# Kernel optimization log

Measured on AMD Instinct MI355X. Metric: run time of the kernel, lower is better.

The kernel has to match this reference:

```python
import jax, jax.numpy as jnp
import numpy as np
from jax import lax

B, H, W = 8, 500, 500
M = 2048          # per-image cap on active bottleneck voxels (ragged -> fixed)
GRID = 125        # bottleneck grid size
ENC_RANGE = 125.0
HEADS, ATTN_CH, CH = 4, 128, 64
EPS = 1e-5
NEG = -1e9

def _conv(x, w, b, stride, pad):
    y = lax.conv_general_dilated(x, w, (stride, stride), pad,
                                 dimension_numbers=('NCHW', 'HWIO', 'NCHW'))
    return y + b[None, :, None, None]

def _maxpool2(m):
    return lax.reduce_window(m, -jnp.inf, lax.max, (1, 1, 2, 2), (1, 1, 2, 2), 'VALID')

def setup_inputs():
    key = jax.random.key(0)
    ks = jax.random.split(key, 12)
    occ = (jax.random.uniform(ks[0], (B, 1, H, W)) < 0.005).astype(jnp.float32)
    x = jax.random.normal(ks[1], (B, 1, H, W), dtype=jnp.float32) * occ
    def rn(k, shape, scale):
        return jax.random.normal(k, shape, dtype=jnp.float32) * scale
    return {
        'x': x,
        'w0': rn(ks[2], (3, 3, 1, 32), 0.3), 'b0': jnp.zeros(32, jnp.float32),
        'g0': jnp.ones(32, jnp.float32), 'be0': jnp.zeros(32, jnp.float32),
        'w1': rn(ks[3], (2, 2, 32, 64), 0.1), 'b1': jnp.zeros(64, jnp.float32),
        'g1': jnp.ones(64, jnp.float32), 'be1': jnp.zeros(64, jnp.float32),
        'w2': rn(ks[4], (2, 2, 64, 64), 0.08), 'b2': jnp.zeros(64, jnp.float32),
        'g2': jnp.ones(64, jnp.float32), 'be2': jnp.zeros(64, jnp.float32),
        'wpe': rn(ks[5], (2, 2, CH), 0.5), 'bpe': jnp.zeros((2, CH), jnp.float32),
        'wq': rn(ks[6], (2, CH, ATTN_CH), 0.12), 'bq': jnp.zeros((2, ATTN_CH), jnp.float32),
        'wk': rn(ks[7], (2, CH, ATTN_CH), 0.12), 'bk': jnp.zeros((2, ATTN_CH), jnp.float32),
        'wv': rn(ks[8], (2, CH, ATTN_CH), 0.12), 'bv': jnp.zeros((2, ATTN_CH), jnp.float32),
        'wo': rn(ks[9], (2, ATTN_CH, CH), 0.09), 'bo': jnp.zeros((2, CH), jnp.float32),
        'wh': rn(ks[10], (CH, 4), 0.12), 'bh': jnp.zeros(4, jnp.float32),
    }

def reference(x, w0, b0, g0, be0, w1, b1, g1, be1, w2, b2, g2, be2,
              wpe, bpe, wq, bq, wk, bk, wv, bv, wo, bo, wh, bh):
    # active-site mask (Voxels.from_dense)
    mask0 = (x != 0).any(axis=1, keepdims=True).astype(x.dtype)   # [B,1,500,500]

    def bn_relu(y, g, be):
        # eval-mode BatchNorm1d over active voxel features (running stats 0/1)
        return jax.nn.relu(g[None, :, None, None] * y / jnp.sqrt(1.0 + EPS)
                           + be[None, :, None, None])

    # enc0: submanifold 3x3/s1 -> active set unchanged; inactive inputs are zero
    y = bn_relu(_conv(x, w0, b0, 1, 'SAME'), g0, be0) * mask0
    # enc1/enc2: strided 2x2/s2 -> output active iff any input in window active
    mask1 = _maxpool2(mask0)
    y = bn_relu(_conv(y, w1, b1, 2, 'VALID'), g1, be1) * mask1
    mask2 = _maxpool2(mask1)
    y = bn_relu(_conv(y, w2, b2, 2, 'VALID'), g2, be2) * mask2    # [B,64,125,125]

    # gather active bottleneck voxels per image (ragged -> fixed M + validity mask)
    mflat = mask2.reshape(B, GRID * GRID)
    vals, idx = lax.top_k(mflat, M)     # active-first; stable tie-break (lowest idx)
    valid = vals                        # [B,M] in {0,1}
    feats = jnp.take_along_axis(
        y.reshape(B, CH, GRID * GRID).transpose(0, 2, 1),
        idx[:, :, None], axis=1)        # [B,M,64]
    pos = jnp.stack([idx // GRID, idx % GRID], axis=-1).astype(x.dtype) / ENC_RANGE

    dh = ATTN_CH // HEADS
    kmask = (1.0 - valid)[:, None, None, :] * NEG
    for i in range(2):  # N_ATTN structurally distinct layers
        pe = pos @ wpe[i] + bpe[i]
        h = feats + pe
        q = (h @ wq[i] + bq[i]).reshape(B, M, HEADS, dh)
        k = (h @ wk[i] + bk[i]).reshape(B, M, HEADS, dh)
        v = (h @ wv[i] + bv[i]).reshape(B, M, HEADS, dh)
        s = jnp.einsum('bqhd,bkhd->bhqk', q, k) / jnp.sqrt(jnp.asarray(dh, x.dtype))
        a = jax.nn.softmax(s + kmask, axis=-1)
        o = jnp.einsum('bhqk,bkhd->bqhd', a, v).reshape(B, M, ATTN_CH)
        feats = (feats + o @ wo[i] + bo[i]) * valid[..., None]

    # sparse_global_avg_pool: mean over active voxels per image
    counts = jnp.clip(valid.sum(axis=1, keepdims=True), 1.0, None)
    pooled = feats.sum(axis=1) / counts                            # [B,64]
    return pooled @ wh + bh                                        # [B,4]
```

## Files before the change

kernel.cpp:

```cpp
#include <hip/hip_runtime.h>

#define BDIM   8
#define NPIX   250000
#define G1N    62500
#define G2N    15625
#define NB0    977
#define NB1    245
#define NB2    62
#define CAP0   4096
#define CAP1   4096
#define CAPM   2048
#define CH     64
#define ACH    128
#define NHEADS 4
#define DH     32
#define KSPLIT 4

static constexpr float BN_INV    = 0.99999500003749969f;
static constexpr float ATT_SCALE = 0.17677669529663687f;

typedef _Float16 f16x8 __attribute__((ext_vector_type(8)));
typedef float f32x4 __attribute__((ext_vector_type(4)));

static constexpr size_t E_MAP0  = 0;
static constexpr size_t E_MAP1  = E_MAP0 + (size_t)BDIM*NPIX;
static constexpr size_t E_CNT   = E_MAP1 + (size_t)BDIM*G1N;
static constexpr size_t E_ZEND  = E_CNT + 32;
static constexpr size_t E_BC    = E_ZEND;
static constexpr size_t E_BO    = E_BC + (size_t)3*BDIM*1024;
static constexpr size_t E_BM    = E_BO + (size_t)3*BDIM*1024;
static constexpr size_t E_LIST0 = E_BM + (size_t)3*BDIM*1024*8;
static constexpr size_t E_LIST1 = E_LIST0 + (size_t)BDIM*CAP0;
static constexpr size_t E_LIST2 = E_LIST1 + (size_t)BDIM*CAP1;
static constexpr size_t E_Y0    = E_LIST2 + (size_t)BDIM*CAPM;
static constexpr size_t E_Y1    = E_Y0 + (size_t)BDIM*CAP0*32;
static constexpr size_t E_FE    = E_Y1 + (size_t)BDIM*CAP1*64;
static constexpr size_t E_QF    = E_FE + (size_t)BDIM*CAPM*64;
static constexpr size_t E_KF    = E_QF + (size_t)32*CAPM*32/2;
static constexpr size_t E_VT    = E_KF + (size_t)32*CAPM*32/2;
static constexpr size_t E_PACC  = E_VT + (size_t)32*CAPM*32/2;
static constexpr size_t E_PML   = E_PACC + (size_t)32*CAPM*KSPLIT*32;
static constexpr size_t E_PART  = E_PML + (size_t)32*CAPM*KSPLIT*2;


__device__ __forceinline__ bool act0(const float* x, int pix, int b) {
  return (pix < NPIX) && (x[(size_t)b * NPIX + pix] != 0.f);
}
__device__ __forceinline__ bool act1(const int* map0, int p, int b) {
  if (p >= G1N) return false;
  int i = p / 250, j = p - i * 250;
  const int* m = map0 + (size_t)b * NPIX + (2 * i) * 500 + 2 * j;
  return (m[0] | m[1] | m[500] | m[501]) != 0;
}
__device__ __forceinline__ bool act2(const int* map1, int p, int b) {
  if (p >= G2N) return false;
  int i = p / 125, j = p - i * 125;
  const int* m = map1 + (size_t)b * G1N + (2 * i) * 250 + 2 * j;
  return (m[0] | m[1] | m[250] | m[251]) != 0;
}

#define COUNT_BODY(ACT_EXPR)                                            \
  int idx = blockIdx.x * 256 + threadIdx.x;                             \
  int b = blockIdx.y;                                                   \
  bool act = (ACT_EXPR);                                                \
  unsigned long long mask = __ballot(act);                              \
  __shared__ int wc[4];                                                 \
  if ((threadIdx.x & 63) == 0) {                                        \
    wc[threadIdx.x >> 6] = __popcll(mask);                              \
    bm[((size_t)b * 1024 + blockIdx.x) * 4 + (threadIdx.x >> 6)] = mask;\
  }                                                                     \
  __syncthreads();                                                      \
  if (threadIdx.x == 0)                                                 \
    bcnt[b * 1024 + blockIdx.x] = wc[0] + wc[1] + wc[2] + wc[3];

__global__ void k_cnt0(const float* __restrict__ x, int* __restrict__ bcnt,
                       unsigned long long* __restrict__ bm) {
  COUNT_BODY(act0(x, idx, b))
}
__global__ void k_cnt1(const int* __restrict__ map0, int* __restrict__ bcnt,
                       unsigned long long* __restrict__ bm) {
  COUNT_BODY(act1(map0, idx, b))
}
__global__ void k_cnt2(const int* __restrict__ map1, int* __restrict__ bcnt,
                       unsigned long long* __restrict__ bm) {
  COUNT_BODY(act2(map1, idx, b))
}

__global__ __launch_bounds__(256) void k_scan(const int* __restrict__ bcnt,
                                              int* __restrict__ boff,
                                              int* __restrict__ cnt,
                                              int nblk, int cbase) {
  int b = blockIdx.x;
  int t = threadIdx.x;
  int base = t * 4;
  int v[4];
  int ts = 0;
#pragma unroll
  for (int u = 0; u < 4; ++u) {
    v[u] = (base + u < nblk) ? bcnt[b * 1024 + base + u] : 0;
    ts += v[u];
  }
  int lane = t & 63, w = t >> 6;
  int incl = ts;
#pragma unroll
  for (int off = 1; off < 64; off <<= 1) {
    int o = __shfl_up(incl, off, 64);
    if (lane >= off) incl += o;
  }
  __shared__ int wsum[4];
  if (lane == 63) wsum[w] = incl;
  __syncthreads();
  int woff = 0;
#pragma unroll
  for (int k = 0; k < 3; ++k) if (k < w) woff += wsum[k];
  int run = woff + incl - ts;
#pragma unroll
  for (int u = 0; u < 4; ++u) {
    if (base + u < nblk) boff[b * 1024 + base + u] = run;
    run += v[u];
  }
  if (t == 255) cnt[cbase + b] = run;
}

#define EMIT_PROLOG                                                     \
  int idx = blockIdx.x * 256 + threadIdx.x;                             \
  int b = blockIdx.y;                                                   \
  int lane = threadIdx.x & 63;                                          \
  unsigned long long mask =                                             \
      bm[((size_t)b * 1024 + blockIdx.x) * 4 + (threadIdx.x >> 6)];     \
  bool act = (mask >> lane) & 1;                                        \
  __shared__ int wbase[4];                                              \
  if (lane == 0) wbase[threadIdx.x >> 6] = __popcll(mask);              \
  __syncthreads();                                                      \
  if (threadIdx.x == 0) {                                               \
    int s = boff[b * 1024 + blockIdx.x];                                \
    for (int w = 0; w < 4; ++w) { int c = wbase[w]; wbase[w] = s; s += c; } \
  }                                                                     \
  __syncthreads();                                                      \
  int slot = wbase[threadIdx.x >> 6] + __popcll(mask & ((1ull << lane) - 1ull));

__global__ void k_emit0(const unsigned long long* __restrict__ bm,
                        const int* __restrict__ boff,
                        int* __restrict__ map0, int* __restrict__ list0) {
  EMIT_PROLOG
  if (act && slot < CAP0) {
    list0[b * CAP0 + slot] = idx;
    map0[(size_t)b * NPIX + idx] = slot + 1;
  }
}
__global__ void k_emit1(const unsigned long long* __restrict__ bm,
                        const int* __restrict__ boff,
                        int* __restrict__ map1, int* __restrict__ list1) {
  EMIT_PROLOG
  if (act && slot < CAP1) {
    list1[b * CAP1 + slot] = idx;
    map1[(size_t)b * G1N + idx] = slot + 1;
  }
}
__global__ void k_emit2(const unsigned long long* __restrict__ bm,
                        const int* __restrict__ boff,
                        int* __restrict__ list2) {
  EMIT_PROLOG
  if (act && slot < CAPM) list2[b * CAPM + slot] = idx;
}


__global__ void k_y0(const float* __restrict__ x, const float* __restrict__ w0,
                     const float* __restrict__ b0, const float* __restrict__ g0,
                     const float* __restrict__ be0,
                     const int* __restrict__ list0, const int* __restrict__ cnt,
                     float* __restrict__ y0) {
  int t = blockIdx.x * 256 + threadIdx.x;
  int b = t >> 17;
  int r = t & 131071;
  int slot = r >> 5, c = r & 31;
  int n = min(cnt[b], CAP0);
  if (slot >= n) return;
  int pix = list0[b * CAP0 + slot];
  int i = pix / 500, j = pix - i * 500;
  float acc = b0[c];
#pragma unroll
  for (int di = 0; di < 3; ++di) {
    int ii = i + di - 1;
    if ((unsigned)ii >= 500u) continue;
#pragma unroll
    for (int dj = 0; dj < 3; ++dj) {
      int jj = j + dj - 1;
      if ((unsigned)jj >= 500u) continue;
      acc += x[(size_t)b * NPIX + ii * 500 + jj] * w0[(di * 3 + dj) * 32 + c];
    }
  }
  float o = g0[c] * acc * BN_INV + be0[c];
  y0[((size_t)(b * CAP0) + slot) * 32 + c] = fmaxf(o, 0.f);
}

__global__ void k_y1(const float* __restrict__ y0, const float* __restrict__ w1,
                     const float* __restrict__ b1, const float* __restrict__ g1,
                     const float* __restrict__ be1,
                     const int* __restrict__ map0, const int* __restrict__ list1,
                     const int* __restrict__ cnt, float* __restrict__ y1) {
  int b = blockIdx.x >> 9;
  int sblk = blockIdx.x & 511;
  int s0 = sblk * 8;
  int n = min(cnt[BDIM + b], CAP1);
  if (s0 >= n) return;
  __shared__ float inT[4][32][8];
  for (int idx = threadIdx.x; idx < 1024; idx += 64) {
    int s = idx & 7;
    int r = idx >> 3;
    int ci = r & 31, pp = r >> 5;
    float v = 0.f;
    int sg = s0 + s;
    if (sg < n) {
      int p = list1[b * CAP1 + sg];
      int i = p / 250, j = p - i * 250;
      int sm = map0[(size_t)b * NPIX + (2 * i + (pp >> 1)) * 500 + (2 * j + (pp & 1))];
      if (sm) v = y0[((size_t)(b * CAP0) + (sm - 1)) * 32 + ci];
    }
    inT[pp][ci][s] = v;
  }
  __syncthreads();
  int co = threadIdx.x;
  float acc[8];
#pragma unroll
  for (int s = 0; s < 8; ++s) acc[s] = b1[co];
#pragma unroll 2
  for (int pp = 0; pp < 4; ++pp)
    for (int ci = 0; ci < 32; ++ci) {
      float wv = w1[((pp << 5) + ci) * 64 + co];
      float4 i0 = *(const float4*)&inT[pp][ci][0];
      float4 i1 = *(const float4*)&inT[pp][ci][4];
      acc[0] += i0.x * wv; acc[1] += i0.y * wv; acc[2] += i0.z * wv; acc[3] += i0.w * wv;
      acc[4] += i1.x * wv; acc[5] += i1.y * wv; acc[6] += i1.z * wv; acc[7] += i1.w * wv;
    }
  int smax = min(8, n - s0);
  for (int s = 0; s < smax; ++s) {
    float o = g1[co] * acc[s] * BN_INV + be1[co];
    y1[((size_t)(b * CAP1) + s0 + s) * 64 + co] = fmaxf(o, 0.f);
  }
}

__global__ void k_y2(const float* __restrict__ y1, const float* __restrict__ w2,
                     const float* __restrict__ b2, const float* __restrict__ g2,
                     const float* __restrict__ be2,
                     const int* __restrict__ map1, const int* __restrict__ list2,
                     const int* __restrict__ cnt, float* __restrict__ feats) {
  int b = blockIdx.x >> 8;
  int sblk = blockIdx.x & 255;
  int s0 = sblk * 8;
  int n = min(cnt[2 * BDIM + b], CAPM);
  if (s0 >= n) return;
  __shared__ float inT[4][64][8];
  for (int idx = threadIdx.x; idx < 2048; idx += 64) {
    int s = idx & 7;
    int r = idx >> 3;
    int ci = r & 63, pp = r >> 6;
    float v = 0.f;
    int sg = s0 + s;
    if (sg < n) {
      int p = list2[b * CAPM + sg];
      int i = p / 125, j = p - i * 125;
      int sm = map1[(size_t)b * G1N + (2 * i + (pp >> 1)) * 250 + (2 * j + (pp & 1))];
      if (sm) v = y1[((size_t)(b * CAP1) + (sm - 1)) * 64 + ci];
    }
    inT[pp][ci][s] = v;
  }
  __syncthreads();
  int co = threadIdx.x;
  float acc[8];
#pragma unroll
  for (int s = 0; s < 8; ++s) acc[s] = b2[co];
#pragma unroll 2
  for (int pp = 0; pp < 4; ++pp)
    for (int ci = 0; ci < 64; ++ci) {
      float wv = w2[((pp << 6) + ci) * 64 + co];
      float4 i0 = *(const float4*)&inT[pp][ci][0];
      float4 i1 = *(const float4*)&inT[pp][ci][4];
      acc[0] += i0.x * wv; acc[1] += i0.y * wv; acc[2] += i0.z * wv; acc[3] += i0.w * wv;
      acc[4] += i1.x * wv; acc[5] += i1.y * wv; acc[6] += i1.z * wv; acc[7] += i1.w * wv;
    }
  int smax = min(8, n - s0);
  for (int s = 0; s < smax; ++s) {
    float o = g2[co] * acc[s] * BN_INV + be2[co];
    feats[((size_t)(b * CAPM) + s0 + s) * 64 + co] = fmaxf(o, 0.f);
  }
}


__global__ void k_qkv(const float* __restrict__ feats, const int* __restrict__ list2,
                      const int* __restrict__ cnt,
                      const float* __restrict__ wpe, const float* __restrict__ bpe,
                      const float* __restrict__ wq, const float* __restrict__ bq,
                      const float* __restrict__ wk, const float* __restrict__ bk,
                      const float* __restrict__ wv, const float* __restrict__ bv,
                      int layer, _Float16* __restrict__ qf, _Float16* __restrict__ kf,
                      _Float16* __restrict__ vt) {
  int b = blockIdx.x & 7;
  int sblk = blockIdx.x >> 3;
  int s0 = sblk * 8;
  int n = min(cnt[2 * BDIM + b], CAPM);
  if (s0 >= n) return;
  __shared__ float hT[64][8];
  for (int idx = threadIdx.x; idx < 512; idx += 128) {
    int s = idx & 7, c = idx >> 3;
    float hv = 0.f;
    int sg = s0 + s;
    if (sg < n) {
      int p = list2[b * CAPM + sg];
      int i = p / 125, j = p - i * 125;
      hv = feats[((size_t)(b * CAPM) + sg) * 64 + c]
         + (float)i * (1.f / 125.f) * wpe[(layer * 2 + 0) * 64 + c]
         + (float)j * (1.f / 125.f) * wpe[(layer * 2 + 1) * 64 + c]
         + bpe[layer * 64 + c];
    }
    hT[c][s] = hv;
  }
  __syncthreads();
  int o = threadIdx.x;
  float accq[8], acck[8], accv[8];
  float bqv = bq[layer * 128 + o], bkv = bk[layer * 128 + o], bvv = bv[layer * 128 + o];
#pragma unroll
  for (int s = 0; s < 8; ++s) { accq[s] = bqv; acck[s] = bkv; accv[s] = bvv; }
  const float* wq_ = wq + (size_t)layer * 64 * 128 + o;
  const float* wk_ = wk + (size_t)layer * 64 * 128 + o;
  const float* wv_ = wv + (size_t)layer * 64 * 128 + o;
  for (int c = 0; c < 64; ++c) {
    float wqv = wq_[c * 128], wkv = wk_[c * 128], wvv = wv_[c * 128];
    float4 h0 = *(const float4*)&hT[c][0];
    float4 h1 = *(const float4*)&hT[c][4];
    float hh[8] = {h0.x, h0.y, h0.z, h0.w, h1.x, h1.y, h1.z, h1.w};
#pragma unroll
    for (int s = 0; s < 8; ++s) {
      accq[s] += hh[s] * wqv; acck[s] += hh[s] * wkv; accv[s] += hh[s] * wvv;
    }
  }
  int hd = o >> 5, d = o & 31;
  size_t bh = (size_t)(b * NHEADS + hd);
  int smax = min(8, n - s0);
  for (int s = 0; s < smax; ++s) {
    size_t rb = (bh * CAPM + s0 + s) * 32 + d;
    qf[rb] = (_Float16)accq[s];
    kf[rb] = (_Float16)acck[s];
    vt[(bh * 32 + d) * CAPM + s0 + s] = (_Float16)accv[s];
  }
}


union U4H8 { uint4 u; f16x8 h; };
union PKU  { _Float16 h[2]; unsigned int u; };

#define LOADK(K0, K1, K2, K3, T0)                                          \
  K0 = *(const f16x8*)(kf + (bh + (T0) + qr) * 32 + g8);                   \
  K1 = *(const f16x8*)(kf + (bh + (T0) + 16 + qr) * 32 + g8);              \
  K2 = *(const f16x8*)(kf + (bh + (T0) + 32 + qr) * 32 + g8);              \
  K3 = *(const f16x8*)(kf + (bh + (T0) + 48 + qr) * 32 + g8);

#define LOADV(V0, V1, V2, V3, T0)                                          \
  V0 = *(const f16x8*)(vbase + (size_t)qr * CAPM + (T0) + g8);             \
  V1 = *(const f16x8*)(vbase + (size_t)(16 + qr) * CAPM + (T0) + g8);      \
  V2 = *(const f16x8*)(vbase + (size_t)qr * CAPM + (T0) + 32 + g8);        \
  V3 = *(const f16x8*)(vbase + (size_t)(16 + qr) * CAPM + (T0) + 32 + g8);

#define PROCESS(K0, K1, K2, K3, V0, V1, V2, V3, T0)                        \
  {                                                                        \
    f32x4 z = {0.f, 0.f, 0.f, 0.f};                                        \
    f32x4 st0 = __builtin_amdgcn_mfma_f32_16x16x32_f16(K0, fq, z, 0, 0, 0);\
    f32x4 st1 = __builtin_amdgcn_mfma_f32_16x16x32_f16(K1, fq, z, 0, 0, 0);\
    f32x4 st2 = __builtin_amdgcn_mfma_f32_16x16x32_f16(K2, fq, z, 0, 0, 0);\
    f32x4 st3 = __builtin_amdgcn_mfma_f32_16x16x32_f16(K3, fq, z, 0, 0, 0);\
    if ((T0) + 64 > n) {                                                   \
      _Pragma("unroll") for (int r = 0; r < 4; ++r) {                      \
        if ((T0) + 4 * g + r >= n)      st0[r] = -1e30f;                   \
        if ((T0) + 16 + 4 * g + r >= n) st1[r] = -1e30f;                   \
        if ((T0) + 32 + 4 * g + r >= n) st2[r] = -1e30f;                   \
        if ((T0) + 48 + 4 * g + r >= n) st3[r] = -1e30f;                   \
      }                                                                    \
    }                                                                      \
    float tm = st0[0];                                                     \
    _Pragma("unroll") for (int r = 1; r < 4; ++r) tm = fmaxf(tm, st0[r]);  \
    _Pragma("unroll") for (int r = 0; r < 4; ++r) tm = fmaxf(tm, st1[r]);  \
    _Pragma("unroll") for (int r = 0; r < 4; ++r) tm = fmaxf(tm, st2[r]);  \
    _Pragma("unroll") for (int r = 0; r < 4; ++r) tm = fmaxf(tm, st3[r]);  \
    tm = fmaxf(tm, __shfl_xor(tm, 16));                                    \
    tm = fmaxf(tm, __shfl_xor(tm, 32));                                    \
    float mn = fmaxf(m, tm * ATT_SCALE);                                   \
    float f_ = __expf(m - mn);                                             \
    m = mn;                                                                \
    float ls = 0.f;                                                        \
    {                                                                      \
      PKU a, c;                                                            \
      a.h[0] = (_Float16)__expf(st0[0] * ATT_SCALE - mn);                  \
      a.h[1] = (_Float16)__expf(st0[1] * ATT_SCALE - mn);                  \
      c.h[0] = (_Float16)__expf(st0[2] * ATT_SCALE - mn);                  \
      c.h[1] = (_Float16)__expf(st0[3] * ATT_SCALE - mn);                  \
      ls += (float)a.h[0] + (float)a.h[1] + (float)c.h[0] + (float)c.h[1]; \
      P[(qr * 32 + 0 + 2 * g) ^ swz] = a.u;                                \
      P[(qr * 32 + 1 + 2 * g) ^ swz] = c.u;                                \
      a.h[0] = (_Float16)__expf(st1[0] * ATT_SCALE - mn);                  \
      a.h[1] = (_Float16)__expf(st1[1] * ATT_SCALE - mn);                  \
      c.h[0] = (_Float16)__expf(st1[2] * ATT_SCALE - mn);                  \
      c.h[1] = (_Float16)__expf(st1[3] * ATT_SCALE - mn);                  \
      ls += (float)a.h[0] + (float)a.h[1] + (float)c.h[0] + (float)c.h[1]; \
      P[(qr * 32 + 8 + 2 * g) ^ swz] = a.u;                                \
      P[(qr * 32 + 9 + 2 * g) ^ swz] = c.u;                                \
      a.h[0] = (_Float16)__expf(st2[0] * ATT_SCALE - mn);                  \
      a.h[1] = (_Float16)__expf(st2[1] * ATT_SCALE - mn);                  \
      c.h[0] = (_Float16)__expf(st2[2] * ATT_SCALE - mn);                  \
      c.h[1] = (_Float16)__expf(st2[3] * ATT_SCALE - mn);                  \
      ls += (float)a.h[0] + (float)a.h[1] + (float)c.h[0] + (float)c.h[1]; \
      P[(qr * 32 + 16 + 2 * g) ^ swz] = a.u;                               \
      P[(qr * 32 + 17 + 2 * g) ^ swz] = c.u;                               \
      a.h[0] = (_Float16)__expf(st3[0] * ATT_SCALE - mn);                  \
      a.h[1] = (_Float16)__expf(st3[1] * ATT_SCALE - mn);                  \
      c.h[0] = (_Float16)__expf(st3[2] * ATT_SCALE - mn);                  \
      c.h[1] = (_Float16)__expf(st3[3] * ATT_SCALE - mn);                  \
      ls += (float)a.h[0] + (float)a.h[1] + (float)c.h[0] + (float)c.h[1]; \
      P[(qr * 32 + 24 + 2 * g) ^ swz] = a.u;                               \
      P[(qr * 32 + 25 + 2 * g) ^ swz] = c.u;                               \
    }                                                                      \
    ls += __shfl_xor(ls, 16);                                              \
    ls += __shfl_xor(ls, 32);                                              \
    l = l * f_ + ls;                                                       \
    __builtin_amdgcn_sched_barrier(0);                                     \
    U4H8 pa0, pa1;                                                         \
    pa0.u = *(const uint4*)&P[(qr * 32 + 4 * g) ^ swz];                    \
    pa1.u = *(const uint4*)&P[(qr * 32 + 16 + 4 * g) ^ swz];               \
    float fr0 = __shfl(f_, 4 * g + 0, 16);                                 \
    float fr1 = __shfl(f_, 4 * g + 1, 16);                                 \
    float fr2 = __shfl(f_, 4 * g + 2, 16);                                 \
    float fr3 = __shfl(f_, 4 * g + 3, 16);                                 \
    acc0[0] *= fr0; acc0[1] *= fr1; acc0[2] *= fr2; acc0[3] *= fr3;        \
    acc1[0] *= fr0; acc1[1] *= fr1; acc1[2] *= fr2; acc1[3] *= fr3;        \
    acc0 = __builtin_amdgcn_mfma_f32_16x16x32_f16(pa0.h, V0, acc0, 0, 0, 0);\
    acc1 = __builtin_amdgcn_mfma_f32_16x16x32_f16(pa0.h, V1, acc1, 0, 0, 0);\
    acc0 = __builtin_amdgcn_mfma_f32_16x16x32_f16(pa1.h, V2, acc0, 0, 0, 0);\
    acc1 = __builtin_amdgcn_mfma_f32_16x16x32_f16(pa1.h, V3, acc1, 0, 0, 0);\
  }

__global__ __launch_bounds__(64, 4) void k_attn(
    const _Float16* __restrict__ qf, const _Float16* __restrict__ kf,
    const _Float16* __restrict__ vt, const int* __restrict__ cnt,
    float* __restrict__ pacc, float* __restrict__ pml) {
  int b  = blockIdx.x & 7;
  int rr = blockIdx.x >> 3;
  int qt = rr & 127;
  rr >>= 7;
  int h  = rr & 3;
  int ks = rr >> 2;
  int n = min(cnt[2 * BDIM + b], CAPM);
  int q0 = qt * 16;
  if (q0 >= n) return;
  int lane = threadIdx.x;
  int g = lane >> 4, qr = lane & 15;
  int g8 = g * 8;
  size_t bh = (size_t)(b * NHEADS + h) * CAPM;
  const _Float16* vbase = vt + (size_t)(b * NHEADS + h) * 32 * CAPM;
  f16x8 fq = *(const f16x8*)(qf + (bh + q0 + qr) * 32 + g8);
  f32x4 acc0 = {0.f, 0.f, 0.f, 0.f}, acc1 = {0.f, 0.f, 0.f, 0.f};
  float m = -1e30f, l = 0.f;
  __shared__ unsigned int P[512];
  int swz = (qr & 7) << 2;

  int nt = (n + 63) >> 6;
  int tpc = (nt + KSPLIT - 1) / KSPLIT;
  int tb = ks * tpc, te = min(nt, tb + tpc);
  if (tb < te) {
    f16x8 ka0, ka1, ka2, ka3, va0, va1, va2, va3;
    f16x8 kb0, kb1, kb2, kb3, vb0, vb1, vb2, vb3;
    LOADK(ka0, ka1, ka2, ka3, tb * 64)
    LOADV(va0, va1, va2, va3, tb * 64)
    for (int t = tb; t < te; t += 2) {
      if (t + 1 < te) {
        LOADK(kb0, kb1, kb2, kb3, (t + 1) * 64)
        LOADV(vb0, vb1, vb2, vb3, (t + 1) * 64)
      }
      PROCESS(ka0, ka1, ka2, ka3, va0, va1, va2, va3, t * 64)
      if (t + 1 < te) {
        if (t + 2 < te) {
          LOADK(ka0, ka1, ka2, ka3, (t + 2) * 64)
          LOADV(va0, va1, va2, va3, (t + 2) * 64)
        }
        PROCESS(kb0, kb1, kb2, kb3, vb0, vb1, vb2, vb3, (t + 1) * 64)
      }
    }
  }
#pragma unroll
  for (int r = 0; r < 4; ++r) {
    int tok = q0 + 4 * g + r;
    if (tok < n) {
      float* pp = pacc + ((bh + tok) * KSPLIT + ks) * 32;
      pp[qr] = acc0[r];
      pp[16 + qr] = acc1[r];
    }
  }
  if (g == 0) {
    int tok = q0 + qr;
    if (tok < n) {
      float* pm = pml + ((bh + tok) * KSPLIT + ks) * 2;
      pm[0] = m; pm[1] = l;
    }
  }
}


__global__ __launch_bounds__(256) void k_cproj(
    const float* __restrict__ pacc, const float* __restrict__ pml,
    const float* __restrict__ wo, const float* __restrict__ bo,
    const int* __restrict__ cnt, int layer, float* __restrict__ feats) {
  int b = blockIdx.x & 7;
  int sblk = blockIdx.x >> 3;
  int s0 = sblk * 4;
  int n = min(cnt[2 * BDIM + b], CAPM);
  if (s0 >= n) return;
  __shared__ float oT[128][4];
  __shared__ float wgt[4][4][4];
  __shared__ float invL[4][4];
  int t = threadIdx.x;
  if (t < 16) {
    int s = t >> 2, h = t & 3;
    const float* pm = pml + (((size_t)(b * NHEADS + h) * CAPM + s0 + s) * KSPLIT) * 2;
    float m0 = pm[0], l0 = pm[1];
    float m1 = pm[2], l1 = pm[3];
    float m2 = pm[4], l2 = pm[5];
    float m3 = pm[6], l3 = pm[7];
    float M = fmaxf(fmaxf(m0, m1), fmaxf(m2, m3));
    float w0_ = __expf(m0 - M), w1_ = __expf(m1 - M);
    float w2_ = __expf(m2 - M), w3_ = __expf(m3 - M);
    float L = w0_ * l0 + w1_ * l1 + w2_ * l2 + w3_ * l3;
    wgt[s][h][0] = w0_; wgt[s][h][1] = w1_;
    wgt[s][h][2] = w2_; wgt[s][h][3] = w3_;
    invL[s][h] = 1.f / L;
  }
  __syncthreads();
#pragma unroll
  for (int k = 0; k < 2; ++k) {
    int id = t + k * 256;
    int c = id >> 2, s = id & 3;
    int h = c >> 5, d = c & 31;
    const float* pp = pacc + (((size_t)(b * NHEADS + h) * CAPM + s0 + s) * KSPLIT) * 32 + d;
    float v = pp[0]  * wgt[s][h][0] + pp[32] * wgt[s][h][1]
            + pp[64] * wgt[s][h][2] + pp[96] * wgt[s][h][3];
    oT[c][s] = v * invL[s][h];
  }
  __syncthreads();
  int s = t >> 6, co = t & 63;
  float acc = bo[layer * 64 + co];
  const float* w = wo + (size_t)layer * 128 * 64 + co;
#pragma unroll 8
  for (int c = 0; c < 128; ++c) acc += oT[c][s] * w[c * 64];
  int tok = s0 + s;
  if (tok < n) feats[((size_t)(b * CAPM) + tok) * 64 + co] += acc;
}


__global__ void k_head1(const float* __restrict__ feats, const int* __restrict__ cnt,
                        float* __restrict__ part) {
  int b = blockIdx.x >> 4;
  int chunk = blockIdx.x & 15;
  int n = min(cnt[2 * BDIM + b], CAPM);
  int c = threadIdx.x & 63, sub = threadIdx.x >> 6;
  int lo = chunk * 128, hi = min(n, lo + 128);
  float s = 0.f;
  for (int mm = lo + sub; mm < hi; mm += 4)
    s += feats[((size_t)(b * CAPM) + mm) * 64 + c];
  __shared__ float red[4][64];
  red[sub][c] = s;
  __syncthreads();
  if (threadIdx.x < 64)
    part[(b * 16 + chunk) * 64 + c] = red[0][c] + red[1][c] + red[2][c] + red[3][c];
}

__global__ void k_head2(const float* __restrict__ part, const float* __restrict__ wh,
                        const float* __restrict__ bhd, const int* __restrict__ cnt,
                        float* __restrict__ out) {
  int b = blockIdx.x;
  int n = min(cnt[2 * BDIM + b], CAPM);
  int c = threadIdx.x;
  float s = 0.f;
#pragma unroll
  for (int k = 0; k < 16; ++k) s += part[(b * 16 + k) * 64 + c];
  __shared__ float pooled[64];
  pooled[c] = s / (float)max(n, 1);
  __syncthreads();
  if (c < 4) {
    float o = bhd[c];
#pragma unroll
    for (int c2 = 0; c2 < 64; ++c2) o += pooled[c2] * wh[c2 * 4 + c];
    out[b * 4 + c] = o;
  }
}


extern "C" void kernel_launch(void* const* d_in, const int* in_sizes, int n_in,
                              void* d_out, int out_size, void* d_ws, size_t ws_size,
                              hipStream_t stream) {
  const float* x   = (const float*)d_in[0];
  const float* w0  = (const float*)d_in[1];
  const float* b0  = (const float*)d_in[2];
  const float* g0  = (const float*)d_in[3];
  const float* be0 = (const float*)d_in[4];
  const float* w1  = (const float*)d_in[5];
  const float* b1  = (const float*)d_in[6];
  const float* g1  = (const float*)d_in[7];
  const float* be1 = (const float*)d_in[8];
  const float* w2  = (const float*)d_in[9];
  const float* b2  = (const float*)d_in[10];
  const float* g2  = (const float*)d_in[11];
  const float* be2 = (const float*)d_in[12];
  const float* wpe = (const float*)d_in[13];
  const float* bpe = (const float*)d_in[14];
  const float* wq  = (const float*)d_in[15];
  const float* bq  = (const float*)d_in[16];
  const float* wk  = (const float*)d_in[17];
  const float* bk  = (const float*)d_in[18];
  const float* wv  = (const float*)d_in[19];
  const float* bv  = (const float*)d_in[20];
  const float* wo  = (const float*)d_in[21];
  const float* bo  = (const float*)d_in[22];
  const float* wh  = (const float*)d_in[23];
  const float* bh  = (const float*)d_in[24];

  int* wsI = (int*)d_ws;
  float* wsF = (float*)d_ws;
  unsigned long long* bm = (unsigned long long*)(wsI + E_BM);
  _Float16* qf = (_Float16*)(wsI + E_QF);
  _Float16* kf = (_Float16*)(wsI + E_KF);
  _Float16* vt = (_Float16*)(wsI + E_VT);

  hipMemsetAsync(d_ws, 0, E_ZEND * 4, stream);

  k_cnt0<<<dim3(NB0, BDIM), 256, 0, stream>>>(x, wsI + E_BC + 0 * BDIM * 1024,
                                              bm + 0 * BDIM * 4096);
  k_scan<<<BDIM, 256, 0, stream>>>(wsI + E_BC + 0 * BDIM * 1024,
                                   wsI + E_BO + 0 * BDIM * 1024,
                                   wsI + E_CNT, NB0, 0);
  k_emit0<<<dim3(NB0, BDIM), 256, 0, stream>>>(bm + 0 * BDIM * 4096,
                                               wsI + E_BO + 0 * BDIM * 1024,
                                               wsI + E_MAP0, wsI + E_LIST0);
  k_y0<<<(BDIM * CAP0 * 32) / 256, 256, 0, stream>>>(
      x, w0, b0, g0, be0, wsI + E_LIST0, wsI + E_CNT, wsF + E_Y0);
  k_cnt1<<<dim3(NB1, BDIM), 256, 0, stream>>>(wsI + E_MAP0,
                                              wsI + E_BC + 1 * BDIM * 1024,
                                              bm + 1 * BDIM * 4096);
  k_scan<<<BDIM, 256, 0, stream>>>(wsI + E_BC + 1 * BDIM * 1024,
                                   wsI + E_BO + 1 * BDIM * 1024,
                                   wsI + E_CNT, NB1, BDIM);
  k_emit1<<<dim3(NB1, BDIM), 256, 0, stream>>>(bm + 1 * BDIM * 4096,
                                               wsI + E_BO + 1 * BDIM * 1024,
                                               wsI + E_MAP1, wsI + E_LIST1);
  k_y1<<<BDIM * (CAP1 / 8), 64, 0, stream>>>(
      wsF + E_Y0, w1, b1, g1, be1, wsI + E_MAP0, wsI + E_LIST1, wsI + E_CNT, wsF + E_Y1);
  k_cnt2<<<dim3(NB2, BDIM), 256, 0, stream>>>(wsI + E_MAP1,
                                              wsI + E_BC + 2 * BDIM * 1024,
                                              bm + 2 * BDIM * 4096);
  k_scan<<<BDIM, 256, 0, stream>>>(wsI + E_BC + 2 * BDIM * 1024,
                                   wsI + E_BO + 2 * BDIM * 1024,
                                   wsI + E_CNT, NB2, 2 * BDIM);
  k_emit2<<<dim3(NB2, BDIM), 256, 0, stream>>>(bm + 2 * BDIM * 4096,
                                               wsI + E_BO + 2 * BDIM * 1024,
                                               wsI + E_LIST2);
  k_y2<<<BDIM * (CAPM / 8), 64, 0, stream>>>(
      wsF + E_Y1, w2, b2, g2, be2, wsI + E_MAP1, wsI + E_LIST2, wsI + E_CNT, wsF + E_FE);

  for (int layer = 0; layer < 2; ++layer) {
    k_qkv<<<BDIM * (CAPM / 8), 128, 0, stream>>>(
        wsF + E_FE, wsI + E_LIST2, wsI + E_CNT, wpe, bpe, wq, bq, wk, bk, wv, bv,
        layer, qf, kf, vt);
    k_attn<<<BDIM * NHEADS * (CAPM / 16) * KSPLIT, 64, 0, stream>>>(
        qf, kf, vt, wsI + E_CNT, wsF + E_PACC, wsF + E_PML);
    k_cproj<<<BDIM * (CAPM / 4), 256, 0, stream>>>(
        wsF + E_PACC, wsF + E_PML, wo, bo, wsI + E_CNT, layer, wsF + E_FE);
  }

  k_head1<<<BDIM * 16, 256, 0, stream>>>(wsF + E_FE, wsI + E_CNT, wsF + E_PART);
  k_head2<<<BDIM, 64, 0, stream>>>(wsF + E_PART, wh, bh, wsI + E_CNT, (float*)d_out);
}
```

Measured before the change: 256.5 us.

## Transpose PV MFMA operands to drop per-step shuffles; merge head kernels

The P·V MFMA now takes V as the A operand and P as the B operand. That makes the accumulator rows line up with the query row each lane already owns, so the per-step rescale uses the lane's own factor f_ and needs no shuffles. The row-sum reduction across lane groups moves out of the inner loop and runs once at the end, and the output stores are rewritten for the new accumulator layout. Separately, the two pooling/head kernels are merged into one 1024-thread block per image, removing a launch and the partial-sum buffer. The risk is that the single-block head reads its rows serially with less parallelism.

```diff
diff --git a/kernel.cpp b/kernel.cpp
--- a/kernel.cpp
+++ b/kernel.cpp
@@ -40,7 +40,6 @@
 static constexpr size_t E_VT    = E_KF + (size_t)32*CAPM*32/2;
 static constexpr size_t E_PACC  = E_VT + (size_t)32*CAPM*32/2;
 static constexpr size_t E_PML   = E_PACC + (size_t)32*CAPM*KSPLIT*32;
-static constexpr size_t E_PART  = E_PML + (size_t)32*CAPM*KSPLIT*2;
 
 
 __device__ __forceinline__ bool act0(const float* x, int pix, int b) {
@@ -418,23 +417,17 @@
       P[(qr * 32 + 24 + 2 * g) ^ swz] = a.u;                               \
       P[(qr * 32 + 25 + 2 * g) ^ swz] = c.u;                               \
     }                                                                      \
-    ls += __shfl_xor(ls, 16);                                              \
-    ls += __shfl_xor(ls, 32);                                              \
     l = l * f_ + ls;                                                       \
     __builtin_amdgcn_sched_barrier(0);                                     \
     U4H8 pa0, pa1;                                                         \
     pa0.u = *(const uint4*)&P[(qr * 32 + 4 * g) ^ swz];                    \
     pa1.u = *(const uint4*)&P[(qr * 32 + 16 + 4 * g) ^ swz];               \
-    float fr0 = __shfl(f_, 4 * g + 0, 16);                                 \
-    float fr1 = __shfl(f_, 4 * g + 1, 16);                                 \
-    float fr2 = __shfl(f_, 4 * g + 2, 16);                                 \
-    float fr3 = __shfl(f_, 4 * g + 3, 16);                                 \
-    acc0[0] *= fr0; acc0[1] *= fr1; acc0[2] *= fr2; acc0[3] *= fr3;        \
-    acc1[0] *= fr0; acc1[1] *= fr1; acc1[2] *= fr2; acc1[3] *= fr3;        \
-    acc0 = __builtin_amdgcn_mfma_f32_16x16x32_f16(pa0.h, V0, acc0, 0, 0, 0);\
-    acc1 = __builtin_amdgcn_mfma_f32_16x16x32_f16(pa0.h, V1, acc1, 0, 0, 0);\
-    acc0 = __builtin_amdgcn_mfma_f32_16x16x32_f16(pa1.h, V2, acc0, 0, 0, 0);\
-    acc1 = __builtin_amdgcn_mfma_f32_16x16x32_f16(pa1.h, V3, acc1, 0, 0, 0);\
+    acc0[0] *= f_; acc0[1] *= f_; acc0[2] *= f_; acc0[3] *= f_;            \
+    acc1[0] *= f_; acc1[1] *= f_; acc1[2] *= f_; acc1[3] *= f_;            \
+    acc0 = __builtin_amdgcn_mfma_f32_16x16x32_f16(V0, pa0.h, acc0, 0, 0, 0);\
+    acc1 = __builtin_amdgcn_mfma_f32_16x16x32_f16(V1, pa0.h, acc1, 0, 0, 0);\
+    acc0 = __builtin_amdgcn_mfma_f32_16x16x32_f16(V2, pa1.h, acc0, 0, 0, 0);\
+    acc1 = __builtin_amdgcn_mfma_f32_16x16x32_f16(V3, pa1.h, acc1, 0, 0, 0);\
   }
 
 __global__ __launch_bounds__(64, 4) void k_attn(
@@ -484,18 +477,17 @@
       }
     }
   }
-#pragma unroll
-  for (int r = 0; r < 4; ++r) {
-    int tok = q0 + 4 * g + r;
-    if (tok < n) {
-      float* pp = pacc + ((bh + tok) * KSPLIT + ks) * 32;
-      pp[qr] = acc0[r];
-      pp[16 + qr] = acc1[r];
-    }
-  }
-  if (g == 0) {
-    int tok = q0 + qr;
-    if (tok < n) {
+  l += __shfl_xor(l, 16);
+  l += __shfl_xor(l, 32);
+  int tok = q0 + qr;
+  if (tok < n) {
+    float* pp = pacc + ((bh + tok) * KSPLIT + ks) * 32;
+#pragma unroll
+    for (int r = 0; r < 4; ++r) {
+      pp[4 * g + r] = acc0[r];
+      pp[16 + 4 * g + r] = acc1[r];
+    }
+    if (g == 0) {
       float* pm = pml + ((bh + tok) * KSPLIT + ks) * 2;
       pm[0] = m; pm[1] = l;
     }
@@ -553,40 +545,33 @@
 }
 
 
-__global__ void k_head1(const float* __restrict__ feats, const int* __restrict__ cnt,
-                        float* __restrict__ part) {
-  int b = blockIdx.x >> 4;
-  int chunk = blockIdx.x & 15;
+__global__ __launch_bounds__(1024) void k_head(
+    const float* __restrict__ feats, const float* __restrict__ wh,
+    const float* __restrict__ bhd, const int* __restrict__ cnt,
+    float* __restrict__ out) {
+  int b = blockIdx.x;
   int n = min(cnt[2 * BDIM + b], CAPM);
-  int c = threadIdx.x & 63, sub = threadIdx.x >> 6;
+  int c = threadIdx.x & 63, chunk = threadIdx.x >> 6;
   int lo = chunk * 128, hi = min(n, lo + 128);
   float s = 0.f;
-  for (int mm = lo + sub; mm < hi; mm += 4)
+  for (int mm = lo; mm < hi; ++mm)
     s += feats[((size_t)(b * CAPM) + mm) * 64 + c];
-  __shared__ float red[4][64];
-  red[sub][c] = s;
-  __syncthreads();
-  if (threadIdx.x < 64)
-    part[(b * 16 + chunk) * 64 + c] = red[0][c] + red[1][c] + red[2][c] + red[3][c];
-}
-
-__global__ void k_head2(const float* __restrict__ part, const float* __restrict__ wh,
-                        const float* __restrict__ bhd, const int* __restrict__ cnt,
-                        float* __restrict__ out) {
-  int b = blockIdx.x;
-  int n = min(cnt[2 * BDIM + b], CAPM);
-  int c = threadIdx.x;
-  float s = 0.f;
-#pragma unroll
-  for (int k = 0; k < 16; ++k) s += part[(b * 16 + k) * 64 + c];
+  __shared__ float red[16][64];
   __shared__ float pooled[64];
-  pooled[c] = s / (float)max(n, 1);
-  __syncthreads();
-  if (c < 4) {
-    float o = bhd[c];
-#pragma unroll
-    for (int c2 = 0; c2 < 64; ++c2) o += pooled[c2] * wh[c2 * 4 + c];
-    out[b * 4 + c] = o;
+  red[chunk][c] = s;
+  __syncthreads();
+  if (threadIdx.x < 64) {
+    float tot = 0.f;
+#pragma unroll
+    for (int k = 0; k < 16; ++k) tot += red[k][c];
+    pooled[c] = tot / (float)max(n, 1);
+  }
+  __syncthreads();
+  if (threadIdx.x < 4) {
+    float o = bhd[threadIdx.x];
+#pragma unroll
+    for (int c2 = 0; c2 < 64; ++c2) o += pooled[c2] * wh[c2 * 4 + threadIdx.x];
+    out[b * 4 + threadIdx.x] = o;
   }
 }
 
@@ -672,6 +657,5 @@
         wsF + E_PACC, wsF + E_PML, wo, bo, wsI + E_CNT, layer, wsF + E_FE);
   }
 
-  k_head1<<<BDIM * 16, 256, 0, stream>>>(wsF + E_FE, wsI + E_CNT, wsF + E_PART);
-  k_head2<<<BDIM, 64, 0, stream>>>(wsF + E_PART, wh, bh, wsI + E_CNT, (float*)d_out);
-}
+  k_head<<<BDIM, 1024, 0, stream>>>(wsF + E_FE, wh, bh, wsI + E_CNT, (float*)d_out);
+}
```

New measurement: 260.9 us. Within noise of the previous version (+1.7%).
